# Performance work log

Hardware: AMD Instinct MI355X
Metric: run time of the kernel (lower is better)

## Reference

```python
import jax, jax.numpy as jnp
import numpy as np

RAD = 4   # corr lookup radius
NH, NP = 8, 4  # deform attn heads / points (single level)


def conv2d(x, w, b, pad):
    y = jax.lax.conv_general_dilated(x, w, (1, 1), [(pad, pad), (pad, pad)],
                                     dimension_numbers=('NCHW', 'OIHW', 'NCHW'))
    return y + b[None, :, None, None]


def bilinear_gather(imgf, H, W, px, py):
    # imgf: [N, C, H*W]; px, py: [N, P] pixel coords; zero padding (grid_sample 'zeros')
    x0 = jnp.floor(px); y0 = jnp.floor(py)
    wx = px - x0; wy = py - y0
    def tap(xi, yi, wt):
        valid = (xi >= 0) & (xi <= W - 1) & (yi >= 0) & (yi <= H - 1)
        idx = (jnp.clip(yi, 0, H - 1) * W + jnp.clip(xi, 0, W - 1)).astype(jnp.int32)
        v = jnp.take_along_axis(imgf, idx[:, None, :], axis=2)
        return v * (wt * valid)[:, None, :]
    return (tap(x0, y0, (1 - wx) * (1 - wy)) + tap(x0 + 1, y0, wx * (1 - wy))
            + tap(x0, y0 + 1, (1 - wx) * wy) + tap(x0 + 1, y0 + 1, wx * wy))


def sine_pos_embed(B, H, W, npf, temperature=10000.0):
    # PositionEmbeddingSine with normalize=True
    scale = 2.0 * np.pi; eps = 1e-6
    y = jnp.broadcast_to(jnp.arange(1, H + 1, dtype=jnp.float32)[:, None], (H, W))
    x = jnp.broadcast_to(jnp.arange(1, W + 1, dtype=jnp.float32)[None, :], (H, W))
    y = (y - 0.5) / (H + eps) * scale
    x = (x - 0.5) / (W + eps) * scale
    dim_t = temperature ** (2.0 * (jnp.arange(npf) // 2).astype(jnp.float32) / npf)
    px = x[..., None] / dim_t
    py = y[..., None] / dim_t
    px = jnp.stack([jnp.sin(px[..., 0::2]), jnp.cos(px[..., 1::2])], -1).reshape(H, W, npf)
    py = jnp.stack([jnp.sin(py[..., 0::2]), jnp.cos(py[..., 1::2])], -1).reshape(H, W, npf)
    pos = jnp.concatenate([py, px], -1)
    return jnp.broadcast_to(pos[None], (B, H, W, 2 * npf)).reshape(B, H * W, 2 * npf)


def layer_norm(x, g, b):
    m = x.mean(-1, keepdims=True)
    v = ((x - m) ** 2).mean(-1, keepdims=True)
    return (x - m) / jnp.sqrt(v + 1e-5) * g + b


def _forward(fmap1, fmap2, flow, wc1, bc1, wc2, bc2, wf1, bf1, wf2, bf2, wcf, bcf,
             wfh1, bfh1, wfh2, bfh2, w_off, b_off, w_aw, b_aw, w_val, b_val,
             w_out, b_out, ln1_g, ln1_b, w_ff1, b_ff1, w_ff2, b_ff2, ln2_g, ln2_b):
    B, C, H, W = fmap1.shape
    HW = H * W
    dh = C // NH
    relu = jax.nn.relu
    # ---- CorrBlock.corr: all-pairs correlation volume ----
    corr = jnp.einsum('bcq,bck->bqk', fmap1.reshape(B, C, HW), fmap2.reshape(B, C, HW))
    corr = corr / jnp.sqrt(jnp.asarray(C, jnp.float32))
    corrf = corr.reshape(B * HW, 1, HW)  # [B*HW, 1, H2*W2]
    # ---- correlation lookup at coords = base grid + flow (bilinear, align_corners=True) ----
    gy, gx = jnp.meshgrid(jnp.arange(H, dtype=jnp.float32),
                          jnp.arange(W, dtype=jnp.float32), indexing='ij')
    cx = (gx[None] + flow[:, 0]).reshape(B * HW)
    cy = (gy[None] + flow[:, 1]).reshape(B * HW)
    d = jnp.linspace(-RAD, RAD, 2 * RAD + 1)
    oy, ox = jnp.meshgrid(d, d, indexing='ij')  # RAFT quirk: delta[...,0]=dy, delta[...,1]=dx
    px = cx[:, None] + oy.reshape(-1)[None, :]
    py = cy[:, None] + ox.reshape(-1)[None, :]
    corr_feat = bilinear_gather(corrf, H, W, px, py).reshape(B, H, W, (2 * RAD + 1) ** 2)
    corr_feat = corr_feat.transpose(0, 3, 1, 2)  # [B, 81, H, W]
    # ---- BasicMotionEncoder + FlowHead (BasicUpdateBlock.forward path) ----
    cor = relu(conv2d(corr_feat, wc1, bc1, 0))
    cor = relu(conv2d(cor, wc2, bc2, 1))
    flo = relu(conv2d(flow, wf1, bf1, 3))
    flo = relu(conv2d(flo, wf2, bf2, 1))
    mf = relu(conv2d(jnp.concatenate([cor, flo], 1), wcf, bcf, 1))
    mf = jnp.concatenate([mf, flow], 1)  # [B,128,H,W]
    delta_flow = conv2d(relu(conv2d(mf, wfh1, bfh1, 1)), wfh2, bfh2, 1)  # [B,2,H,W]
    # ---- single-level MSDeformAttn encoder layer over fmap1 tokens ----
    src = fmap1.reshape(B, C, HW).transpose(0, 2, 1)  # [B, Lq, C]
    pos = sine_pos_embed(B, H, W, C // 2)
    q = src + pos
    off = (q @ w_off.T + b_off).reshape(B, HW, NH, 1, NP, 2)
    aw = jax.nn.softmax((q @ w_aw.T + b_aw).reshape(B, HW, NH, NP), axis=-1)
    val = (src @ w_val.T + b_val).reshape(B, HW, NH, dh)
    ref = jnp.stack([(gx.reshape(-1) + 0.5) / W, (gy.reshape(-1) + 0.5) / H], -1)  # [HW,2]
    loc = (ref[None, :, None, None, None, :] + off / jnp.asarray([W, H], jnp.float32))[:, :, :, 0]
    # normalized loc -> pixel coords with align_corners=False convention
    px2 = (loc[..., 0] * W - 0.5).transpose(0, 2, 1, 3).reshape(B * NH, HW * NP)
    py2 = (loc[..., 1] * H - 0.5).transpose(0, 2, 1, 3).reshape(B * NH, HW * NP)
    vflat = val.transpose(0, 2, 3, 1).reshape(B * NH, dh, HW)
    samp = bilinear_gather(vflat, H, W, px2, py2).reshape(B, NH, dh, HW, NP)
    attn = (samp * aw.transpose(0, 2, 1, 3)[:, :, None]).sum(-1)  # [B,NH,dh,HW]
    attn = attn.transpose(0, 3, 1, 2).reshape(B, HW, C) @ w_out.T + b_out
    src = layer_norm(src + attn, ln1_g, ln1_b)
    ff = jax.nn.relu(src @ w_ff1.T + b_ff1) @ w_ff2.T + b_ff2
    src = layer_norm(src + ff, ln2_g, ln2_b)
    return src, delta_flow


def setup_inputs():
    key = jax.random.key(0)
    ks = jax.random.split(key, 20)
    B, C, H, W = 4, 256, 48, 48
    def w(i, shape, s=0.02):
        return jax.random.normal(ks[i], shape, jnp.float32) * s
    return {
        'fmap1': jax.random.normal(ks[0], (B, C, H, W), jnp.float32),
        'fmap2': jax.random.normal(ks[1], (B, C, H, W), jnp.float32),
        'flow': jax.random.normal(ks[2], (B, 2, H, W), jnp.float32),
        'wc1': w(3, (256, 81, 1, 1)), 'bc1': jnp.zeros((256,)),
        'wc2': w(4, (192, 256, 3, 3)), 'bc2': jnp.zeros((192,)),
        'wf1': w(5, (128, 2, 7, 7)), 'bf1': jnp.zeros((128,)),
        'wf2': w(6, (64, 128, 3, 3)), 'bf2': jnp.zeros((64,)),
        'wcf': w(7, (126, 256, 3, 3)), 'bcf': jnp.zeros((126,)),
        'wfh1': w(8, (256, 128, 3, 3)), 'bfh1': jnp.zeros((256,)),
        'wfh2': w(9, (2, 256, 3, 3)), 'bfh2': jnp.zeros((2,)),
        'w_off': w(10, (64, 256)), 'b_off': jnp.zeros((64,)),
        'w_aw': w(11, (32, 256)), 'b_aw': jnp.zeros((32,)),
        'w_val': w(12, (256, 256)), 'b_val': jnp.zeros((256,)),
        'w_out': w(13, (256, 256)), 'b_out': jnp.zeros((256,)),
        'ln1_g': jnp.ones((256,)), 'ln1_b': jnp.zeros((256,)),
        'w_ff1': w(14, (1024, 256)), 'b_ff1': jnp.zeros((1024,)),
        'w_ff2': w(15, (256, 1024)), 'b_ff2': jnp.zeros((256,)),
        'ln2_g': jnp.ones((256,)), 'ln2_b': jnp.zeros((256,)),
    }


def reference(fmap1, fmap2, flow, wc1, bc1, wc2, bc2, wf1, bf1, wf2, bf2, wcf, bcf,
              wfh1, bfh1, wfh2, bfh2, w_off, b_off, w_aw, b_aw, w_val, b_val,
              w_out, b_out, ln1_g, ln1_b, w_ff1, b_ff1, w_ff2, b_ff2, ln2_g, ln2_b):
    return _forward(fmap1, fmap2, flow, wc1, bc1, wc2, bc2, wf1, bf1, wf2, bf2, wcf, bcf,
                    wfh1, bfh1, wfh2, bfh2, w_off, b_off, w_aw, b_aw, w_val, b_val,
                    w_out, b_out, ln1_g, ln1_b, w_ff1, b_ff1, w_ff2, b_ff2, ln2_g, ln2_b)
```

## Files before the change

### kernel.cpp

```cpp
#include <hip/hip_runtime.h>
#include <hip/hip_bf16.h>
#include <math.h>

#define HH 48
#define WW 48
#define HW 2304
#define BB 4
#define CC 256

typedef __hip_bfloat16 bf16;
typedef __attribute__((ext_vector_type(8))) short s8v;
typedef __attribute__((ext_vector_type(4))) float f4v;

__device__ inline float bf2f(short u) {
  unsigned v = ((unsigned)(unsigned short)u) << 16;
  return __builtin_bit_cast(float, v);
}

__global__ __launch_bounds__(256) void prep_k(const float* __restrict__ fmap1,
                                              const float* __restrict__ fmap2,
                                              float* __restrict__ srcT,
                                              bf16* __restrict__ f1t,
                                              bf16* __restrict__ qb,
                                              bf16* __restrict__ f2t) {
  __shared__ float t[64][65];
  int z = blockIdx.z;
  int p0 = blockIdx.x * 64, c0 = blockIdx.y * 64;
  int b = z & 3;
  const float* src = (z < 4) ? fmap2 : fmap1;
  const float* inb = src + ((size_t)b * CC + c0) * HW + p0;
#pragma unroll
  for (int i = 0; i < 16; ++i) {
    int idx = threadIdx.x + i * 256;
    int c = idx >> 6, p = idx & 63;
    t[c][p] = inb[(size_t)c * HW + p];
  }
  __syncthreads();
  if (z < 4) {
    bf16* ob = f2t + ((size_t)b * HW + p0) * 256 + c0;
#pragma unroll
    for (int i = 0; i < 16; ++i) {
      int idx = threadIdx.x + i * 256;
      int p = idx >> 6, c = idx & 63;
      ob[(size_t)p * 256 + c] = (bf16)t[c][p];
    }
  } else {
    const float TWO_PI = 6.283185307179586f;
#pragma unroll
    for (int i = 0; i < 16; ++i) {
      int idx = threadIdx.x + i * 256;
      int pl = idx >> 6, cl = idx & 63;
      int c = c0 + cl;
      int p = p0 + pl;
      int y = p / WW, x = p % WW;
      float s = t[cl][pl];
      int axis = c >> 7;
      int cc = c & 127;
      int mm = cc >> 1;
      float coord = (axis ? ((float)x + 0.5f) : ((float)y + 0.5f)) * (TWO_PI / (48.f + 1e-6f));
      float tp = exp2f((float)mm * (13.287712379549449f / 64.f));
      float a = coord / tp;
      float pv = (cc & 1) ? cosf(a) : sinf(a);
      size_t o = ((size_t)b * HW + p) * 256 + c;
      srcT[o] = s;
      f1t[o] = (bf16)s;
      qb[o] = (bf16)(s + pv);
    }
  }
}

__global__ __launch_bounds__(256) void corr_mfma_k(const bf16* __restrict__ f1t,
                                                   const bf16* __restrict__ f2t,
                                                   bf16* __restrict__ corr) {
  int b = blockIdx.z;
  int m0 = blockIdx.y * 128, n0 = blockIdx.x * 64;
  __shared__ short smem[12288];
  short* As = smem;
  short* Bs = smem + 128 * 64;
  int tid = threadIdx.x;
  int arl = tid >> 1, asl = (tid & 1) * 4;
  int brl = tid >> 2, bsl = (tid & 3) * 2;
  int wave = tid >> 6, lane = tid & 63;
  int wm = (wave >> 1) * 64, wn = (wave & 1) * 32;
  int fl = lane & 15, fk8 = lane >> 4;
  f4v acc[4][2] = {};
  const bf16* arow = f1t + ((size_t)b * HW + m0 + arl) * 256;
  const bf16* brow = f2t + ((size_t)b * HW + n0 + brl) * 256;
  uint4 apre[4], bpre[2];
#pragma unroll
  for (int q = 0; q < 4; ++q) apre[q] = *(const uint4*)(arow + (asl + q) * 8);
#pragma unroll
  for (int q = 0; q < 2; ++q) bpre[q] = *(const uint4*)(brow + (bsl + q) * 8);
  for (int st = 0; st < 4; ++st) {
#pragma unroll
    for (int q = 0; q < 4; ++q) {
      int sr = asl + q;
      *(uint4*)&As[arl * 64 + ((sr ^ (arl & 7))) * 8] = apre[q];
    }
#pragma unroll
    for (int q = 0; q < 2; ++q) {
      int sr = bsl + q;
      *(uint4*)&Bs[brl * 64 + ((sr ^ (brl & 7))) * 8] = bpre[q];
    }
    if (st < 3) {
      int c0 = (st + 1) * 64;
#pragma unroll
      for (int q = 0; q < 4; ++q) apre[q] = *(const uint4*)(arow + c0 + (asl + q) * 8);
#pragma unroll
      for (int q = 0; q < 2; ++q) bpre[q] = *(const uint4*)(brow + c0 + (bsl + q) * 8);
    }
    __syncthreads();
#pragma unroll
    for (int cc = 0; cc < 2; ++cc) {
      s8v af[4], bfr[2];
#pragma unroll
      for (int i = 0; i < 4; ++i) {
        int ar = wm + i * 16 + fl;
        af[i] = *(const s8v*)&As[ar * 64 + (((cc * 4 + fk8) ^ (ar & 7))) * 8];
      }
#pragma unroll
      for (int j = 0; j < 2; ++j) {
        int br = wn + j * 16 + fl;
        bfr[j] = *(const s8v*)&Bs[br * 64 + (((cc * 4 + fk8) ^ (br & 7))) * 8];
      }
#pragma unroll
      for (int i = 0; i < 4; ++i)
#pragma unroll
        for (int j = 0; j < 2; ++j)
          acc[i][j] = __builtin_amdgcn_mfma_f32_16x16x32_bf16(af[i], bfr[j], acc[i][j], 0, 0, 0);
    }
    __syncthreads();
  }
  bf16* Cs = (bf16*)smem;
#pragma unroll
  for (int j = 0; j < 2; ++j) {
    int o = wn + j * 16 + fl;
#pragma unroll
    for (int i = 0; i < 4; ++i)
#pragma unroll
      for (int r = 0; r < 4; ++r) {
        int m = wm + i * 16 + fk8 * 4 + r;
        Cs[m * 80 + o] = (bf16)(acc[i][j][r] * 0.0625f);
      }
  }
  __syncthreads();
  bf16* outp = corr + ((size_t)b * HW + m0) * HW + n0;
#pragma unroll
  for (int it = 0; it < 4; ++it) {
    int gi = it * 256 + tid;
    int r = gi >> 3, ch = gi & 7;
    uint4 v = *(const uint4*)&Cs[r * 80 + ch * 8];
    *(uint4*)(outp + (size_t)r * HW + ch * 8) = v;
  }
}

__global__ __launch_bounds__(256) void corr_lookup_k(const bf16* __restrict__ corr,
                                                     const float* __restrict__ flow,
                                                     bf16* __restrict__ cf) {
  int g = blockIdx.x * 256 + threadIdx.x;
  int t = g % 96;
  int n = g / 96;
  if (t >= 81) { cf[g] = (bf16)0.f; return; }
  int b = n / HW;
  int p = n % HW;
  int y = p / WW, x = p % WW;
  float fx = flow[((size_t)b * 2 + 0) * HW + p];
  float fy = flow[((size_t)b * 2 + 1) * HW + p];
  float px = (float)x + fx + (float)(t / 9 - 4);
  float py = (float)y + fy + (float)(t % 9 - 4);
  const bf16* row = corr + (size_t)n * HW;
  float x0f = floorf(px), y0f = floorf(py);
  int x0 = (int)x0f, y0 = (int)y0f;
  float wx = px - x0f, wy = py - y0f;
  float acc = 0.f;
  if ((unsigned)x0 < WW && (unsigned)y0 < HH) acc += (float)row[y0 * WW + x0] * (1.f - wx) * (1.f - wy);
  if ((unsigned)(x0 + 1) < WW && (unsigned)y0 < HH) acc += (float)row[y0 * WW + x0 + 1] * wx * (1.f - wy);
  if ((unsigned)x0 < WW && (unsigned)(y0 + 1) < HH) acc += (float)row[(y0 + 1) * WW + x0] * (1.f - wx) * wy;
  if ((unsigned)(x0 + 1) < WW && (unsigned)(y0 + 1) < HH) acc += (float)row[(y0 + 1) * WW + x0 + 1] * wx * wy;
  cf[g] = (bf16)acc;
}

struct WtSegs {
  const float* src[12];
  unsigned dstOff[12];
  int Cout[12], Cin[12], KP[12], KS2[12];
  unsigned cum[13];
};

__global__ __launch_bounds__(256) void wt_all_k(WtSegs s, bf16* __restrict__ base) {
  unsigned idx = blockIdx.x * 256 + threadIdx.x;
  if (idx >= s.cum[12]) return;
  int seg = 0;
#pragma unroll
  for (int i = 1; i < 12; ++i)
    if (idx >= s.cum[i]) seg = i;
  unsigned r = idx - s.cum[seg];
  int KP = s.KP[seg], Cout = s.Cout[seg], Cin = s.Cin[seg], KS2 = s.KS2[seg];
  int c = r % KP;
  int o = (r / KP) % Cout;
  int t = r / (KP * Cout);
  float v;
  if (KS2 == 0) {
    int cc = c >> 6, tt = c & 63;
    v = (tt < 49) ? s.src[seg][((size_t)o * 2 + cc) * 49 + tt] : 0.f;
  } else {
    v = (c < Cin) ? s.src[seg][((size_t)o * Cin + c) * KS2 + t] : 0.f;
  }
  base[s.dstOff[seg] + r] = (bf16)v;
}

__global__ __launch_bounds__(256) void im2col7_k(const float* __restrict__ flow,
                                                 bf16* __restrict__ col7) {
  int g = blockIdx.x * 256 + threadIdx.x;
  int kp = g & 127;
  int n = g >> 7;
  int b = n / HW;
  int p = n % HW;
  int y = p / WW, x = p % WW;
  int cc = kp >> 6, tt = kp & 63;
  float v = 0.f;
  if (tt < 49) {
    int ky = tt / 7, kx = tt % 7;
    int yy = y + ky - 3, xx = x + kx - 3;
    if ((unsigned)yy < (unsigned)HH && (unsigned)xx < (unsigned)WW)
      v = flow[((size_t)b * 2 + cc) * HW + yy * WW + xx];
  }
  col7[g] = (bf16)v;
}

struct GSegs {
  const bf16* in[4];
  const bf16* wt[4];
  const float* bias[4];
  const float* bias2[4];
  float* outf[4];
  bf16* outb[4];
  int split[4], O[4], KP[4], taps[4], OStride[4], OOff[4], relu[4], nTn[4];
  int blkStart[4];
  int nseg;
};

__global__ __launch_bounds__(256) void gemm_group_k(GSegs s) {
  int blk = blockIdx.x;
  int seg = 0;
#pragma unroll
  for (int i = 1; i < 4; ++i)
    if (i < s.nseg && blk >= s.blkStart[i]) seg = i;
  int rel = blk - s.blkStart[seg];
  int nTn = s.nTn[seg];
  int bm = rel / nTn, bn = rel % nTn;
  int m0 = bm * 128, n0 = bn * 64;
  int KP = s.KP[seg], O = s.O[seg], taps = s.taps[seg];
  const bf16* in = s.in[seg];
  const bf16* wt = s.wt[seg];

  __shared__ short As[2][128][64];
  __shared__ short Bs[2][64][64];
  int tid = threadIdx.x;
  int arl = tid >> 1, asl = (tid & 1) * 4;
  int brl = tid >> 2, bsl = (tid & 3) * 2;
  int wave = tid >> 6, lane = tid & 63;
  int wm = (wave >> 1) * 64, wn = (wave & 1) * 32;
  int fl = lane & 15, fk8 = lane >> 4;
  f4v acc[4][2] = {};
  int m = m0 + arl;
  int b = m / HW;
  int p = m - b * HW;
  int y = p / WW, x = p - y * WW;
  int wo = n0 + brl;
  bool wvalid = wo < O;
  int wo_c = wvalid ? wo : 0;

  int nc0 = (KP + 63) >> 6;
  int S = taps * nc0;
  uint4 apre[4], bpre[2];

  auto load_stage = [&](int st) {
    int t = st / nc0;
    int c0 = (st - t * nc0) * 64;
    int yy = y, xx = x;
    bool valid = true;
    if (taps == 9) {
      int ky = t / 3, kx = t - ky * 3;
      yy = y + ky - 1;
      xx = x + kx - 1;
      valid = ((unsigned)yy < (unsigned)HH) & ((unsigned)xx < (unsigned)WW);
    }
    const bf16* arow = in + ((size_t)b * HW + yy * WW + xx) * KP;
    const bf16* wrow = wt + ((size_t)t * O + wo_c) * KP;
#pragma unroll
    for (int q = 0; q < 4; ++q) {
      int col = c0 + (asl + q) * 8;
      uint4 v = {0u, 0u, 0u, 0u};
      if (valid && col < KP) v = *(const uint4*)(arow + col);
      apre[q] = v;
    }
#pragma unroll
    for (int q = 0; q < 2; ++q) {
      int col = c0 + (bsl + q) * 8;
      uint4 v = {0u, 0u, 0u, 0u};
      if (wvalid && col < KP) v = *(const uint4*)(wrow + col);
      bpre[q] = v;
    }
  };

  load_stage(0);
  int cur = 0;
  for (int st = 0; st < S; ++st) {
#pragma unroll
    for (int q = 0; q < 4; ++q) {
      int sr = asl + q;
      *(uint4*)&As[cur][arl][((sr ^ (arl & 7))) * 8] = apre[q];
    }
#pragma unroll
    for (int q = 0; q < 2; ++q) {
      int sr = bsl + q;
      *(uint4*)&Bs[cur][brl][((sr ^ (brl & 7))) * 8] = bpre[q];
    }
    if (st + 1 < S) load_stage(st + 1);
    __syncthreads();
#pragma unroll
    for (int cc = 0; cc < 2; ++cc) {
      s8v af[4], bfr[2];
#pragma unroll
      for (int i = 0; i < 4; ++i) {
        int ar = wm + i * 16 + fl;
        af[i] = *(const s8v*)&As[cur][ar][(((cc * 4 + fk8) ^ (ar & 7))) * 8];
      }
#pragma unroll
      for (int j = 0; j < 2; ++j) {
        int br = wn + j * 16 + fl;
        bfr[j] = *(const s8v*)&Bs[cur][br][(((cc * 4 + fk8) ^ (br & 7))) * 8];
      }
#pragma unroll
      for (int i = 0; i < 4; ++i)
#pragma unroll
        for (int j = 0; j < 2; ++j)
          acc[i][j] = __builtin_amdgcn_mfma_f32_16x16x32_bf16(af[i], bfr[j], acc[i][j], 0, 0, 0);
    }
    cur ^= 1;
  }
  int OStride = s.OStride[seg], OOff = s.OOff[seg], relu = s.relu[seg], split = s.split[seg];
  const float* bias = s.bias[seg];
  const float* bias2 = s.bias2[seg];
  float* outf = s.outf[seg];
  bf16* outb = s.outb[seg];
#pragma unroll
  for (int j = 0; j < 2; ++j) {
    int o = n0 + wn + j * 16 + fl;
    if (o < O) {
      float bsv = (bias2 != nullptr && o >= split) ? bias2[o - split] : bias[o];
#pragma unroll
      for (int i = 0; i < 4; ++i)
#pragma unroll
        for (int r = 0; r < 4; ++r) {
          int mm = m0 + wm + i * 16 + fk8 * 4 + r;
          float v = acc[i][j][r] + bsv;
          if (relu) v = fmaxf(v, 0.f);
          if (outb) outb[(size_t)mm * OStride + OOff + o] = (bf16)v;
          else outf[(size_t)mm * OStride + OOff + o] = v;
        }
    }
  }
}

__global__ __launch_bounds__(256) void convfh2_k(const bf16* __restrict__ fh1,
                                                 const float* __restrict__ w,
                                                 const float* __restrict__ bias,
                                                 float* __restrict__ out) {
  __shared__ float wl[4608];
  int tid = threadIdx.x;
#pragma unroll
  for (int i = tid; i < 4608; i += 256) {
    int o2 = i & 1;
    int t = (i >> 1) % 9;
    int c = i / 18;
    wl[i] = w[((size_t)o2 * 256 + c) * 9 + t];
  }
  __syncthreads();
  int wave = tid >> 6, lane = tid & 63;
  int pix = blockIdx.x * 4 + wave;
  int b = pix / HW;
  int q = pix % HW;
  int y = q / WW, x = q % WW;
  int c0 = lane * 4;
  float a0 = 0.f, a1 = 0.f;
#pragma unroll
  for (int ky = 0; ky < 3; ++ky) {
    int yy = y + ky - 1;
    if ((unsigned)yy >= (unsigned)HH) continue;
#pragma unroll
    for (int kx = 0; kx < 3; ++kx) {
      int xx = x + kx - 1;
      if ((unsigned)xx >= (unsigned)WW) continue;
      int t = ky * 3 + kx;
      const bf16* row = fh1 + ((size_t)b * HW + yy * WW + xx) * 256 + c0;
      ushort4 v = *(const ushort4*)row;
      unsigned short vv[4] = {v.x, v.y, v.z, v.w};
#pragma unroll
      for (int j = 0; j < 4; ++j) {
        float fv = bf2f((short)vv[j]);
        float2 wp = *(const float2*)&wl[((c0 + j) * 9 + t) * 2];
        a0 += fv * wp.x;
        a1 += fv * wp.y;
      }
    }
  }
#pragma unroll
  for (int offl = 32; offl > 0; offl >>= 1) {
    a0 += __shfl_xor(a0, offl);
    a1 += __shfl_xor(a1, offl);
  }
  if (lane == 0) {
    out[(size_t)b * 2 * HW + q] = a0 + bias[0];
    out[((size_t)b * 2 + 1) * HW + q] = a1 + bias[1];
  }
}

__global__ void copy_flow_k(const float* __restrict__ flow, bf16* __restrict__ mf) {
  int g = blockIdx.x * 256 + threadIdx.x;
  int p = g % HW;
  int c = (g / HW) % 2;
  int b = g / (2 * HW);
  mf[((size_t)b * HW + p) * 128 + 126 + c] = (bf16)flow[g];
}

__global__ __launch_bounds__(256) void deform_k(const float* __restrict__ val,
                                                const float* __restrict__ oa,
                                                bf16* __restrict__ attn) {
  int g = blockIdx.x * 256 + threadIdx.x;
  int d = g & 31;
  int nh = g >> 5;
  int h = nh & 7;
  int n = nh >> 3;
  int b = n / HW;
  int p = n % HW;
  int y = p / WW, x = p % WW;
  const float* ap = oa + (size_t)n * 96 + 64 + h * 4;
  float l0 = ap[0], l1 = ap[1], l2 = ap[2], l3 = ap[3];
  float mx = fmaxf(fmaxf(l0, l1), fmaxf(l2, l3));
  float e0 = expf(l0 - mx), e1 = expf(l1 - mx), e2 = expf(l2 - mx), e3 = expf(l3 - mx);
  float inv = 1.f / (e0 + e1 + e2 + e3);
  float wts[4] = {e0 * inv, e1 * inv, e2 * inv, e3 * inv};
  const float* offp = oa + (size_t)n * 96 + h * 8;
  const float* vb = val + (size_t)b * HW * 256 + h * 32 + d;
  float acc = 0.f;
#pragma unroll
  for (int pt = 0; pt < 4; ++pt) {
    float ox = offp[pt * 2 + 0];
    float oy = offp[pt * 2 + 1];
    float w = wts[pt];
    float px = (float)x + ox, py = (float)y + oy;
    float x0f = floorf(px), y0f = floorf(py);
    int x0 = (int)x0f, y0 = (int)y0f;
    float wx = px - x0f, wy = py - y0f;
    float s = 0.f;
    if ((unsigned)x0 < WW && (unsigned)y0 < HH)
      s += vb[(size_t)(y0 * WW + x0) * 256] * (1.f - wx) * (1.f - wy);
    if ((unsigned)(x0 + 1) < WW && (unsigned)y0 < HH)
      s += vb[(size_t)(y0 * WW + x0 + 1) * 256] * wx * (1.f - wy);
    if ((unsigned)x0 < WW && (unsigned)(y0 + 1) < HH)
      s += vb[(size_t)((y0 + 1) * WW + x0) * 256] * (1.f - wx) * wy;
    if ((unsigned)(x0 + 1) < WW && (unsigned)(y0 + 1) < HH)
      s += vb[(size_t)((y0 + 1) * WW + x0 + 1) * 256] * wx * wy;
    acc += w * s;
  }
  attn[(size_t)n * 256 + h * 32 + d] = (bf16)acc;
}

__global__ __launch_bounds__(256) void ln_add_k(const float* __restrict__ A,
                                                const float* __restrict__ Bv,
                                                const float* __restrict__ g,
                                                const float* __restrict__ be,
                                                float* __restrict__ out,
                                                bf16* __restrict__ outb) {
  int n = blockIdx.x;
  int c = threadIdx.x;
  float v = A[(size_t)n * 256 + c] + Bv[(size_t)n * 256 + c];
  float s1 = v, s2 = v * v;
#pragma unroll
  for (int o = 32; o > 0; o >>= 1) {
    s1 += __shfl_down(s1, o);
    s2 += __shfl_down(s2, o);
  }
  __shared__ float r1[4], r2[4], mv[2];
  int wid = c >> 6, lane = c & 63;
  if (lane == 0) {
    r1[wid] = s1;
    r2[wid] = s2;
  }
  __syncthreads();
  if (c == 0) {
    float a = r1[0] + r1[1] + r1[2] + r1[3];
    float q2 = r2[0] + r2[1] + r2[2] + r2[3];
    float mean = a * (1.f / 256.f);
    mv[0] = mean;
    mv[1] = q2 * (1.f / 256.f) - mean * mean;
  }
  __syncthreads();
  float mean = mv[0], var = mv[1];
  float r = (v - mean) * rsqrtf(var + 1e-5f) * g[c] + be[c];
  out[(size_t)n * 256 + c] = r;
  if (outb) outb[(size_t)n * 256 + c] = (bf16)r;
}

extern "C" void kernel_launch(void* const* d_in, const int* in_sizes, int n_in,
                              void* d_out, int out_size, void* d_ws, size_t ws_size,
                              hipStream_t stream) {
  const float* fmap1 = (const float*)d_in[0];
  const float* fmap2 = (const float*)d_in[1];
  const float* flow = (const float*)d_in[2];
  const float* wc1 = (const float*)d_in[3];
  const float* bc1 = (const float*)d_in[4];
  const float* wc2 = (const float*)d_in[5];
  const float* bc2 = (const float*)d_in[6];
  const float* wf1 = (const float*)d_in[7];
  const float* bf1 = (const float*)d_in[8];
  const float* wf2 = (const float*)d_in[9];
  const float* bf2 = (const float*)d_in[10];
  const float* wcf = (const float*)d_in[11];
  const float* bcf = (const float*)d_in[12];
  const float* wfh1 = (const float*)d_in[13];
  const float* bfh1 = (const float*)d_in[14];
  const float* wfh2 = (const float*)d_in[15];
  const float* bfh2 = (const float*)d_in[16];
  const float* w_off = (const float*)d_in[17];
  const float* b_off = (const float*)d_in[18];
  const float* w_aw = (const float*)d_in[19];
  const float* b_aw = (const float*)d_in[20];
  const float* w_val = (const float*)d_in[21];
  const float* b_val = (const float*)d_in[22];
  const float* w_out = (const float*)d_in[23];
  const float* b_out = (const float*)d_in[24];
  const float* ln1_g = (const float*)d_in[25];
  const float* ln1_b = (const float*)d_in[26];
  const float* w_ff1 = (const float*)d_in[27];
  const float* b_ff1 = (const float*)d_in[28];
  const float* w_ff2 = (const float*)d_in[29];
  const float* b_ff2 = (const float*)d_in[30];
  const float* ln2_g = (const float*)d_in[31];
  const float* ln2_b = (const float*)d_in[32];

  float* ws = (float*)d_ws;
  float* out_src = (float*)d_out;
  float* out_df = out_src + (size_t)BB * HW * CC;

  const size_t F_WT = 0;
  const size_t F_CORR = 1000000;
  const size_t F_F1T = 11700000;
  const size_t F_F2T = 12900000;
  const size_t F_QB = 14100000;
  const size_t F_SRCT = 15300000;
  const size_t F_CF = 17700000;
  const size_t F_COL7 = 18200000;
  const size_t F_COR1 = 18800000;
  const size_t F_FLO1 = 20000000;
  const size_t F_CAT = 20600000;
  const size_t F_MF = 21800000;
  const size_t F_FH1 = 22400000;
  const size_t F_OA = 23600000;
  const size_t F_VAL = 24500000;
  const size_t F_ATTN = 26900000;
  const size_t F_TMP = 28100000;
  const size_t F_SRC1 = 30500000;
  const size_t F_SRC1B = 32900000;
  const size_t F_FF1 = 34100000;
  const size_t F_FF2 = 38900000;

  bf16* wkbase = (bf16*)(ws + F_WT);
  bf16* wk1 = wkbase + 0;
  bf16* wk2 = wkbase + 24576;
  bf16* wkf2 = wkbase + 466944;
  bf16* wkcf = wkbase + 540672;
  bf16* wkfh1 = wkbase + 830976;
  bf16* wl_oa = wkbase + 1125888;
  bf16* wl_val = wkbase + 1150464;
  bf16* wl_out = wkbase + 1216000;
  bf16* wl_ff1 = wkbase + 1281536;
  bf16* wl_ff2 = wkbase + 1543680;
  bf16* wk7 = wkbase + 1805824;
  bf16* corrb = (bf16*)(ws + F_CORR);
  bf16* f1t = (bf16*)(ws + F_F1T);
  bf16* f2t = (bf16*)(ws + F_F2T);
  bf16* qb = (bf16*)(ws + F_QB);
  bf16* cf = (bf16*)(ws + F_CF);
  bf16* col7 = (bf16*)(ws + F_COL7);
  bf16* cor1 = (bf16*)(ws + F_COR1);
  bf16* flo1 = (bf16*)(ws + F_FLO1);
  bf16* cat = (bf16*)(ws + F_CAT);
  bf16* mf = (bf16*)(ws + F_MF);
  bf16* fh1 = (bf16*)(ws + F_FH1);
  bf16* attnb = (bf16*)(ws + F_ATTN);
  bf16* src1b = (bf16*)(ws + F_SRC1B);
  bf16* ff1b = (bf16*)(ws + F_FF1);

  WtSegs segs;
  const float* srcs[12] = {wc1, wc2, wf2, wcf, wfh1, w_off, w_aw, w_val, w_out, w_ff1, w_ff2, wf1};
  unsigned offs[12] = {0, 24576, 466944, 540672, 830976, 1125888, 1142272, 1150464, 1216000, 1281536, 1543680, 1805824};
  int couts[12] = {256, 192, 64, 126, 256, 64, 32, 256, 256, 1024, 256, 128};
  int cins[12] = {81, 256, 128, 256, 128, 256, 256, 256, 256, 256, 1024, 2};
  int kps[12] = {96, 256, 128, 256, 128, 256, 256, 256, 256, 256, 1024, 128};
  int ks2[12] = {1, 9, 9, 9, 9, 1, 1, 1, 1, 1, 1, 0};
  unsigned cum = 0;
  for (int i = 0; i < 12; ++i) {
    segs.src[i] = srcs[i];
    segs.dstOff[i] = offs[i];
    segs.Cout[i] = couts[i];
    segs.Cin[i] = cins[i];
    segs.KP[i] = kps[i];
    segs.KS2[i] = ks2[i];
    segs.cum[i] = cum;
    cum += (unsigned)((ks2[i] ? ks2[i] : 1) * couts[i] * kps[i]);
  }
  segs.cum[12] = cum;
  wt_all_k<<<dim3((cum + 255) / 256), 256, 0, stream>>>(segs, wkbase);

  prep_k<<<dim3(36, 4, 8), 256, 0, stream>>>(fmap1, fmap2, ws + F_SRCT, f1t, qb, f2t);
  im2col7_k<<<dim3(4608), 256, 0, stream>>>(flow, col7);
  copy_flow_k<<<dim3(72), 256, 0, stream>>>(flow, mf);

  corr_mfma_k<<<dim3(36, 18, 4), 256, 0, stream>>>(f1t, f2t, corrb);
  corr_lookup_k<<<dim3(3456), 256, 0, stream>>>(corrb, flow, cf);

  auto setseg = [](GSegs& G, int i, const bf16* in, const bf16* wt, const float* bias,
                   const float* bias2, int split, float* outf, bf16* outb, int O, int KP,
                   int taps, int OStride, int OOff, int relu) {
    G.in[i] = in; G.wt[i] = wt; G.bias[i] = bias; G.bias2[i] = bias2; G.split[i] = split;
    G.outf[i] = outf; G.outb[i] = outb; G.O[i] = O; G.KP[i] = KP; G.taps[i] = taps;
    G.OStride[i] = OStride; G.OOff[i] = OOff; G.relu[i] = relu;
    G.nTn[i] = (O + 63) / 64;
  };
  auto finseg = [](GSegs& G, int n) {
    int cumb = 0;
    for (int i = 0; i < 4; ++i) {
      if (i < n) { G.blkStart[i] = cumb; cumb += G.nTn[i] * 72; }
      else G.blkStart[i] = 0x7fffffff;
    }
    G.nseg = n;
    return cumb;
  };

  GSegs GA;
  setseg(GA, 0, cf, wk1, bc1, nullptr, 1 << 30, nullptr, cor1, 256, 96, 1, 256, 0, 1);
  setseg(GA, 1, col7, wk7, bf1, nullptr, 1 << 30, nullptr, flo1, 128, 128, 1, 128, 0, 1);
  setseg(GA, 2, qb, wl_oa, b_off, b_aw, 64, ws + F_OA, nullptr, 96, 256, 1, 96, 0, 0);
  setseg(GA, 3, f1t, wl_val, b_val, nullptr, 1 << 30, ws + F_VAL, nullptr, 256, 256, 1, 256, 0, 0);
  int nblkA = finseg(GA, 4);
  gemm_group_k<<<dim3(nblkA), 256, 0, stream>>>(GA);

  deform_k<<<dim3(9216), 256, 0, stream>>>(ws + F_VAL, ws + F_OA, attnb);

  GSegs GB;
  setseg(GB, 0, cor1, wk2, bc2, nullptr, 1 << 30, nullptr, cat, 192, 256, 9, 256, 0, 1);
  setseg(GB, 1, flo1, wkf2, bf2, nullptr, 1 << 30, nullptr, cat, 64, 128, 9, 256, 192, 1);
  setseg(GB, 2, attnb, wl_out, b_out, nullptr, 1 << 30, ws + F_TMP, nullptr, 256, 256, 1, 256, 0, 0);
  int nblkB = finseg(GB, 3);
  gemm_group_k<<<dim3(nblkB), 256, 0, stream>>>(GB);

  ln_add_k<<<dim3(9216), 256, 0, stream>>>(ws + F_TMP, ws + F_SRCT, ln1_g, ln1_b, ws + F_SRC1, src1b);

  GSegs GC;
  setseg(GC, 0, cat, wkcf, bcf, nullptr, 1 << 30, nullptr, mf, 126, 256, 9, 128, 0, 1);
  setseg(GC, 1, src1b, wl_ff1, b_ff1, nullptr, 1 << 30, nullptr, ff1b, 1024, 256, 1, 1024, 0, 1);
  int nblkC = finseg(GC, 2);
  gemm_group_k<<<dim3(nblkC), 256, 0, stream>>>(GC);

  GSegs GD;
  setseg(GD, 0, mf, wkfh1, bfh1, nullptr, 1 << 30, nullptr, fh1, 256, 128, 9, 256, 0, 1);
  setseg(GD, 1, ff1b, wl_ff2, b_ff2, nullptr, 1 << 30, ws + F_FF2, nullptr, 256, 1024, 1, 256, 0, 0);
  int nblkD = finseg(GD, 2);
  gemm_group_k<<<dim3(nblkD), 256, 0, stream>>>(GD);

  convfh2_k<<<dim3(2304), 256, 0, stream>>>(fh1, wfh2, bfh2, out_df);
  ln_add_k<<<dim3(9216), 256, 0, stream>>>(ws + F_FF2, ws + F_SRC1, ln2_g, ln2_b, out_src, nullptr);

  (void)in_sizes; (void)n_in; (void)out_size; (void)ws_size;
}
```

Baseline: 284.3 us.

## Enlarge correlation GEMM tile to 128x128 and remap blocks across XCDs

```diff
diff --git a/kernel.cpp b/kernel.cpp
--- a/kernel.cpp
+++ b/kernel.cpp
@@ -72,84 +72,83 @@
 __global__ __launch_bounds__(256) void corr_mfma_k(const bf16* __restrict__ f1t,
                                                    const bf16* __restrict__ f2t,
                                                    bf16* __restrict__ corr) {
-  int b = blockIdx.z;
-  int m0 = blockIdx.y * 128, n0 = blockIdx.x * 64;
-  __shared__ short smem[12288];
+  __shared__ short smem[17408];
   short* As = smem;
-  short* Bs = smem + 128 * 64;
+  short* Bs = smem + 8192;
+  int blk = blockIdx.x;
+  int lg = (blk & 7) * 162 + (blk >> 3);
+  int nx = lg % 18;
+  int rem = lg / 18;
+  int my = rem % 18;
+  int b = rem / 18;
+  int m0 = my * 128, n0 = nx * 128;
   int tid = threadIdx.x;
-  int arl = tid >> 1, asl = (tid & 1) * 4;
-  int brl = tid >> 2, bsl = (tid & 3) * 2;
+  int srl = tid >> 1, ssl = (tid & 1) * 4;
   int wave = tid >> 6, lane = tid & 63;
-  int wm = (wave >> 1) * 64, wn = (wave & 1) * 32;
+  int wm = (wave >> 1) * 64, wn = (wave & 1) * 64;
   int fl = lane & 15, fk8 = lane >> 4;
-  f4v acc[4][2] = {};
-  const bf16* arow = f1t + ((size_t)b * HW + m0 + arl) * 256;
-  const bf16* brow = f2t + ((size_t)b * HW + n0 + brl) * 256;
-  uint4 apre[4], bpre[2];
-#pragma unroll
-  for (int q = 0; q < 4; ++q) apre[q] = *(const uint4*)(arow + (asl + q) * 8);
-#pragma unroll
-  for (int q = 0; q < 2; ++q) bpre[q] = *(const uint4*)(brow + (bsl + q) * 8);
+  f4v acc[4][4] = {};
+  const bf16* arow = f1t + ((size_t)b * HW + m0 + srl) * 256;
+  const bf16* brow = f2t + ((size_t)b * HW + n0 + srl) * 256;
+  uint4 apre[4], bpre[4];
+#pragma unroll
+  for (int q = 0; q < 4; ++q) {
+    apre[q] = *(const uint4*)(arow + (ssl + q) * 8);
+    bpre[q] = *(const uint4*)(brow + (ssl + q) * 8);
+  }
   for (int st = 0; st < 4; ++st) {
 #pragma unroll
     for (int q = 0; q < 4; ++q) {
-      int sr = asl + q;
-      *(uint4*)&As[arl * 64 + ((sr ^ (arl & 7))) * 8] = apre[q];
-    }
-#pragma unroll
-    for (int q = 0; q < 2; ++q) {
-      int sr = bsl + q;
-      *(uint4*)&Bs[brl * 64 + ((sr ^ (brl & 7))) * 8] = bpre[q];
+      int sr = ssl + q;
+      *(uint4*)&As[srl * 64 + ((sr ^ (srl & 7))) * 8] = apre[q];
+      *(uint4*)&Bs[srl * 64 + ((sr ^ (srl & 7))) * 8] = bpre[q];
     }
     if (st < 3) {
       int c0 = (st + 1) * 64;
 #pragma unroll
-      for (int q = 0; q < 4; ++q) apre[q] = *(const uint4*)(arow + c0 + (asl + q) * 8);
-#pragma unroll
-      for (int q = 0; q < 2; ++q) bpre[q] = *(const uint4*)(brow + c0 + (bsl + q) * 8);
+      for (int q = 0; q < 4; ++q) {
+        apre[q] = *(const uint4*)(arow + c0 + (ssl + q) * 8);
+        bpre[q] = *(const uint4*)(brow + c0 + (ssl + q) * 8);
+      }
     }
     __syncthreads();
 #pragma unroll
     for (int cc = 0; cc < 2; ++cc) {
-      s8v af[4], bfr[2];
+      s8v af[4], bfr[4];
 #pragma unroll
       for (int i = 0; i < 4; ++i) {
         int ar = wm + i * 16 + fl;
         af[i] = *(const s8v*)&As[ar * 64 + (((cc * 4 + fk8) ^ (ar & 7))) * 8];
+        int br = wn + i * 16 + fl;
+        bfr[i] = *(const s8v*)&Bs[br * 64 + (((cc * 4 + fk8) ^ (br & 7))) * 8];
       }
 #pragma unroll
-      for (int j = 0; j < 2; ++j) {
-        int br = wn + j * 16 + fl;
-        bfr[j] = *(const s8v*)&Bs[br * 64 + (((cc * 4 + fk8) ^ (br & 7))) * 8];
-      }
-#pragma unroll
       for (int i = 0; i < 4; ++i)
 #pragma unroll
-        for (int j = 0; j < 2; ++j)
+        for (int j = 0; j < 4; ++j)
           acc[i][j] = __builtin_amdgcn_mfma_f32_16x16x32_bf16(af[i], bfr[j], acc[i][j], 0, 0, 0);
     }
     __syncthreads();
   }
   bf16* Cs = (bf16*)smem;
 #pragma unroll
-  for (int j = 0; j < 2; ++j) {
+  for (int j = 0; j < 4; ++j) {
     int o = wn + j * 16 + fl;
 #pragma unroll
     for (int i = 0; i < 4; ++i)
 #pragma unroll
       for (int r = 0; r < 4; ++r) {
         int m = wm + i * 16 + fk8 * 4 + r;
-        Cs[m * 80 + o] = (bf16)(acc[i][j][r] * 0.0625f);
+        Cs[m * 136 + o] = (bf16)(acc[i][j][r] * 0.0625f);
       }
   }
   __syncthreads();
   bf16* outp = corr + ((size_t)b * HW + m0) * HW + n0;
 #pragma unroll
-  for (int it = 0; it < 4; ++it) {
+  for (int it = 0; it < 8; ++it) {
     int gi = it * 256 + tid;
-    int r = gi >> 3, ch = gi & 7;
-    uint4 v = *(const uint4*)&Cs[r * 80 + ch * 8];
+    int r = gi >> 4, ch = gi & 15;
+    uint4 v = *(const uint4*)&Cs[r * 136 + ch * 8];
     *(uint4*)(outp + (size_t)r * HW + ch * 8) = v;
   }
 }
@@ -619,7 +618,7 @@
   im2col7_k<<<dim3(4608), 256, 0, stream>>>(flow, col7);
   copy_flow_k<<<dim3(72), 256, 0, stream>>>(flow, mf);
 
-  corr_mfma_k<<<dim3(36, 18, 4), 256, 0, stream>>>(f1t, f2t, corrb);
+  corr_mfma_k<<<dim3(1296), 256, 0, stream>>>(f1t, f2t, corrb);
   corr_lookup_k<<<dim3(3456), 256, 0, stream>>>(corrb, flow, cf);
 
   auto setseg = [](GSegs& G, int i, const bf16* in, const bf16* wt, const float* bias,
```

Measured after the change: 288.4 us. About the same (+1.4%).
